# Optimization experiments

Hardware: AMD Instinct MI355X
Metric: run time of the kernel (lower is better)

The kernel has to match this reference:

```python
import jax, jax.numpy as jnp
import numpy as np

D_MODEL = 64
NUM_MODES = 16
SCALE = 1.0 / (D_MODEL * D_MODEL)


def setup_inputs() -> dict:
    key = jax.random.key(0)
    kq, kk, kv = jax.random.split(key, 3)
    shape = (4, 2048, 64, 64)  # (b, t, c, mw_dim)
    q = jax.random.normal(kq, shape, dtype=jnp.float32)
    k = jax.random.normal(kk, shape, dtype=jnp.float32)
    v = jax.random.normal(kv, shape, dtype=jnp.float32)
    return {"q": q, "k": k, "v": v}


def reference(q, k, v):
    b, t, c, mw = q.shape
    modes = min(t // 2, NUM_MODES)
    # permute (b,t,c,mw) -> (b,h,d,t) with h=mw_dim, d=c
    xq = jnp.transpose(q, (0, 3, 2, 1))
    xk = jnp.transpose(k, (0, 3, 2, 1))
    xv = jnp.transpose(v, (0, 3, 2, 1))
    # rfft over time, keep lowest `modes` frequency bins (contiguous low-pass)
    qf = jnp.fft.rfft(xq, axis=-1)[..., :modes]  # (b,h,d,modes) complex64
    kf = jnp.fft.rfft(xk, axis=-1)[..., :modes]
    vf = jnp.fft.rfft(xv, axis=-1)[..., :modes]
    # complex-domain attention over the reduced mode set
    qk = jnp.einsum('bhdx,bhdy->bhxy', qf, kf)  # (b,h,modes,modes)
    qk = jnp.tanh(qk)  # complex tanh, matching torch.tanh on cfloat
    qkv = jnp.einsum('bhxy,bhdy->bhdx', qk, vf)  # (b,h,d,modes)
    # scatter back into full rfft spectrum (zeros elsewhere)
    out_ft = jnp.zeros((b, mw, c, t // 2 + 1), dtype=qkv.dtype)
    out_ft = out_ft.at[..., :modes].set(qkv)
    out = jnp.fft.irfft(out_ft * SCALE, n=t, axis=-1)  # (b,h,d,t) float32
    return jnp.transpose(out, (0, 3, 2, 1))  # (b,t,c,mw)
```

## Files before the change

kernel.cpp:

```cpp
#include <hip/hip_runtime.h>
#include <hip/hip_bf16.h>
#include <math.h>


#define B_DIM 4
#define T_DIM 2048
#define DH 4096
#define MODES 16
#define CHUNKS 8
#define TPC (1024 / CHUNKS)

__global__ void init_tables(float* __restrict__ Wt, float* __restrict__ Bt) {
    int i = blockIdx.x * 256 + threadIdx.x;
    const float TWO_PI = 6.2831853071795864769f;
    if (i < 1024 * 32) {
        int t = i >> 5, j = i & 31, m = j & 15;
        int ph = (m * t) & 2047;
        float ang = TWO_PI * (float)ph / 2048.0f;
        Wt[i] = (j < 16) ? cosf(ang) : sinf(ang);
    }
    int i2 = i - 1024 * 32;
    if (i2 >= 0 && i2 < 2048 * 32) {
        int t = i2 >> 5, j = i2 & 31, m = j & 15;
        int ph = (m * t) & 2047;
        float ang = TWO_PI * (float)ph / 2048.0f;
        const float S2 = 1.0f / (4096.0f * 2048.0f);
        float coef = (m == 0 ? 1.0f : 2.0f) * S2;
        float val;
        if (j < 16)      val = coef * cosf(ang);
        else if (m == 0) val = 0.0f;
        else             val = -coef * sinf(ang);
        Bt[i2] = val;
    }
}

__global__ __launch_bounds__(256) void stageA(
        const float* __restrict__ q, const float* __restrict__ k,
        const float* __restrict__ v, const float* __restrict__ Wt,
        float* __restrict__ P) {
    int tid = threadIdx.x;
    int dh  = blockIdx.x * 256 + tid;
    int c   = blockIdx.y;
    int tz  = blockIdx.z;
    int tensor = tz >> 2;
    int b      = tz & 3;
    const float* src = (tensor == 0 ? q : tensor == 1 ? k : v)
                       + (size_t)b * T_DIM * DH;
    float accC[16], accS[16];
    #pragma unroll
    for (int m = 0; m < 16; m++) { accC[m] = 0.f; accS[m] = 0.f; }

    int t0 = c * TPC;
    const float* s0 = src + (size_t)t0 * DH + dh;
    const float* s1 = s0 + (size_t)1024 * DH;
    const float* wr0 = Wt + (size_t)t0 * 32;

    #pragma unroll 2
    for (int tl = 0; tl < TPC; tl++) {
        float x0 = s0[(size_t)tl * DH];
        float x1 = s1[(size_t)tl * DH];
        float u = x0 + x1;
        float w = x0 - x1;
        const float* wr = wr0 + tl * 32;
        #pragma unroll
        for (int m = 0; m < 16; m++) {
            float sm = (m & 1) ? w : u;
            accC[m] = fmaf(wr[m],      sm, accC[m]);
            accS[m] = fmaf(wr[16 + m], sm, accS[m]);
        }
    }
    float* pp = P + (((size_t)tz * CHUNKS + c) * 32) * DH + dh;
    #pragma unroll
    for (int m = 0; m < 16; m++) {
        pp[(size_t)m * DH]        = accC[m];
        pp[(size_t)(16 + m) * DH] = -accS[m];
    }
}

__global__ __launch_bounds__(256) void reduceP(const float* __restrict__ P,
                                               float* __restrict__ Y) {
    size_t i   = (size_t)blockIdx.x * 256 + threadIdx.x;
    size_t tzj = i >> 12;
    size_t dh  = i & 4095;
    size_t tz  = tzj >> 5;
    size_t j   = tzj & 31;
    const float* p = P + ((tz * CHUNKS) * 32 + j) * DH + dh;
    float s = 0.f;
    #pragma unroll
    for (int cc = 0; cc < CHUNKS; cc++) s += p[(size_t)cc * 32 * DH];
    Y[i] = s;
}

__global__ __launch_bounds__(256) void stageB(const float* __restrict__ Y,
                                              float* __restrict__ G) {
    __shared__ float qf[64 * 33];
    __shared__ float kf[64 * 33];
    __shared__ float vf[64 * 33];
    __shared__ float qkr[16 * 17];
    __shared__ float qki[16 * 17];

    int tid = threadIdx.x;
    int bh  = blockIdx.x;
    int b   = bh >> 6;
    int h   = bh & 63;

    #pragma unroll
    for (int tensor = 0; tensor < 3; tensor++) {
        float* dst = (tensor == 0 ? qf : tensor == 1 ? kf : vf);
        const float* yp = Y + ((size_t)(tensor * 4 + b) * 32) * DH + h;
        #pragma unroll
        for (int it = 0; it < 8; it++) {
            int p = it * 256 + tid;
            int d = p & 63, j = p >> 6;
            dst[d * 33 + j] = yp[(size_t)j * DH + d * 64];
        }
    }
    __syncthreads();

    int x = tid >> 4, y = tid & 15;
    float ar = 0.f, ai = 0.f;
    #pragma unroll 4
    for (int d = 0; d < 64; d++) {
        float qr = qf[d * 33 + x],      qi = qf[d * 33 + 16 + x];
        float kr = kf[d * 33 + y],      ki = kf[d * 33 + 16 + y];
        ar += qr * kr - qi * ki;
        ai += qr * ki + qi * kr;
    }
    float re, im;
    float a2 = 2.f * ar, b2 = 2.f * ai;
    if (fabsf(a2) < 80.f) {
        float den = coshf(a2) + cosf(b2);
        re = sinhf(a2) / den;
        im = sinf(b2) / den;
    } else {
        re = copysignf(1.f, ar);
        im = 0.f;
    }
    qkr[x * 17 + y] = re;
    qki[x * 17 + y] = im;
    __syncthreads();

    int xx = tid & 15, db = tid >> 4;
    #pragma unroll
    for (int i = 0; i < 4; i++) {
        int d = db + i * 16;
        float cr = 0.f, ci = 0.f;
        #pragma unroll
        for (int yy = 0; yy < 16; yy++) {
            float tr = qkr[xx * 17 + yy], ti = qki[xx * 17 + yy];
            float vr = vf[d * 33 + yy],   vi = vf[d * 33 + 16 + yy];
            cr += tr * vr - ti * vi;
            ci += tr * vi + ti * vr;
        }
        G[((size_t)b * 32 + xx) * DH + d * 64 + h]      = cr;
        G[((size_t)b * 32 + 16 + xx) * DH + d * 64 + h] = ci;
    }
}

__global__ __launch_bounds__(256) void stageC(const float* __restrict__ G,
                                              const float* __restrict__ Bt,
                                              float* __restrict__ out) {
    int tid   = threadIdx.x;
    int dh    = blockIdx.x * 256 + tid;
    int ttile = blockIdx.y;
    int b     = blockIdx.z;

    float g[32];
    const float* gp = G + (size_t)b * 32 * DH + dh;
    #pragma unroll
    for (int j = 0; j < 32; j++) g[j] = gp[(size_t)j * DH];

    float* op = out + ((size_t)b * T_DIM + (size_t)ttile * 128) * DH + dh;
    const float* bp = Bt + (size_t)ttile * 128 * 32;
    for (int tl = 0; tl < 128; tl++) {
        float acc = 0.f;
        #pragma unroll
        for (int j = 0; j < 32; j++) acc = fmaf(bp[tl * 32 + j], g[j], acc);
        op[(size_t)tl * DH] = acc;
    }
}

extern "C" void kernel_launch(void* const* d_in, const int* in_sizes, int n_in,
                              void* d_out, int out_size, void* d_ws, size_t ws_size,
                              hipStream_t stream) {
    const float* q = (const float*)d_in[0];
    const float* k = (const float*)d_in[1];
    const float* v = (const float*)d_in[2];
    float* out = (float*)d_out;

    char* ws = (char*)d_ws;
    float* Wt = (float*)ws;
    float* Bt = (float*)(ws + 131072);
    float* P  = (float*)(ws + 131072 + 262144);
    float* Y  = (float*)(ws + 131072 + 262144 + 50331648);
    float* G  = (float*)(ws + 131072 + 262144 + 50331648 + 6291456);

    init_tables<<<384, 256, 0, stream>>>(Wt, Bt);
    stageA<<<dim3(16, CHUNKS, 12), 256, 0, stream>>>(q, k, v, Wt, P);
    reduceP<<<6144, 256, 0, stream>>>(P, Y);
    stageB<<<256, 256, 0, stream>>>(Y, G);
    stageC<<<dim3(16, 16, 4), 256, 0, stream>>>(G, Bt, out);
}
```

Baseline: 463.9 us.

## Use radix-4 time folding, float2 vectorization and LDS twiddle tables in DFT stages

The forward DFT stage now folds the time axis four ways, using the periodicity of the low modes (m mod 4). This cuts the twiddle FMAs per sample, and each thread processes two channels with float2 loads. Twiddle tables are staged in shared memory rather than read from global memory, and the reduction kernel is vectorized to float4. The inverse stage uses even/odd mode symmetry to produce outputs at t and t+1024 from one accumulation, which halves its table work. In exchange, register pressure rises from float2 accumulators, there are fewer blocks, and the stage-A chunk length is shorter.

```diff
diff --git a/kernel.cpp b/kernel.cpp
--- a/kernel.cpp
+++ b/kernel.cpp
@@ -3,91 +3,124 @@
 #include <math.h>
 
 
-#define B_DIM 4
 #define T_DIM 2048
 #define DH 4096
-#define MODES 16
-#define CHUNKS 8
-#define TPC (1024 / CHUNKS)
-
-__global__ void init_tables(float* __restrict__ Wt, float* __restrict__ Bt) {
+#define DH2 2048
+#define CH 8
+#define TPCH 64
+#define TT 32
+
+__global__ void init_tables(float* __restrict__ WA, float* __restrict__ Bt2) {
     int i = blockIdx.x * 256 + threadIdx.x;
     const float TWO_PI = 6.2831853071795864769f;
-    if (i < 1024 * 32) {
-        int t = i >> 5, j = i & 31, m = j & 15;
+    if (i < 512 * 32) {
+        int t = i >> 5, r = i & 31, m = r >> 1;
         int ph = (m * t) & 2047;
-        float ang = TWO_PI * (float)ph / 2048.0f;
-        Wt[i] = (j < 16) ? cosf(ang) : sinf(ang);
-    }
-    int i2 = i - 1024 * 32;
-    if (i2 >= 0 && i2 < 2048 * 32) {
-        int t = i2 >> 5, j = i2 & 31, m = j & 15;
+        float ang = TWO_PI * (float)ph * (1.0f / 2048.0f);
+        WA[i] = (r & 1) ? sinf(ang) : cosf(ang);
+    }
+    int i2 = i - 512 * 32;
+    if (i2 >= 0 && i2 < 1024 * 32) {
+        int t = i2 >> 5, r = i2 & 31, m = r >> 1;
         int ph = (m * t) & 2047;
-        float ang = TWO_PI * (float)ph / 2048.0f;
+        float ang = TWO_PI * (float)ph * (1.0f / 2048.0f);
         const float S2 = 1.0f / (4096.0f * 2048.0f);
         float coef = (m == 0 ? 1.0f : 2.0f) * S2;
         float val;
-        if (j < 16)      val = coef * cosf(ang);
-        else if (m == 0) val = 0.0f;
-        else             val = -coef * sinf(ang);
-        Bt[i2] = val;
+        if (!(r & 1)) val = coef * cosf(ang);
+        else          val = (m == 0) ? 0.0f : -coef * sinf(ang);
+        Bt2[i2] = val;
     }
 }
 
 __global__ __launch_bounds__(256) void stageA(
         const float* __restrict__ q, const float* __restrict__ k,
-        const float* __restrict__ v, const float* __restrict__ Wt,
+        const float* __restrict__ v, const float* __restrict__ WA,
         float* __restrict__ P) {
+    __shared__ float w[TPCH * 32];
     int tid = threadIdx.x;
-    int dh  = blockIdx.x * 256 + tid;
     int c   = blockIdx.y;
     int tz  = blockIdx.z;
-    int tensor = tz >> 2;
-    int b      = tz & 3;
-    const float* src = (tensor == 0 ? q : tensor == 1 ? k : v)
-                       + (size_t)b * T_DIM * DH;
-    float accC[16], accS[16];
-    #pragma unroll
-    for (int m = 0; m < 16; m++) { accC[m] = 0.f; accS[m] = 0.f; }
-
-    int t0 = c * TPC;
-    const float* s0 = src + (size_t)t0 * DH + dh;
-    const float* s1 = s0 + (size_t)1024 * DH;
-    const float* wr0 = Wt + (size_t)t0 * 32;
+    int tensor = tz >> 2, b = tz & 3;
+
+    #pragma unroll
+    for (int it = 0; it < TPCH * 32 / 256; it++)
+        w[it * 256 + tid] = WA[c * (TPCH * 32) + it * 256 + tid];
+    __syncthreads();
+
+    int dh2 = blockIdx.x * 256 + tid;
+    const float* srcf = (tensor == 0 ? q : tensor == 1 ? k : v)
+                        + (size_t)b * T_DIM * DH;
+    const float2* p0 = (const float2*)srcf + (size_t)(c * TPCH) * DH2 + dh2;
+
+    float2 accR[16], accI[16];
+    #pragma unroll
+    for (int m = 0; m < 16; m++) {
+        accR[m] = make_float2(0.f, 0.f);
+        accI[m] = make_float2(0.f, 0.f);
+    }
 
     #pragma unroll 2
-    for (int tl = 0; tl < TPC; tl++) {
-        float x0 = s0[(size_t)tl * DH];
-        float x1 = s1[(size_t)tl * DH];
-        float u = x0 + x1;
-        float w = x0 - x1;
-        const float* wr = wr0 + tl * 32;
+    for (int tl = 0; tl < TPCH; tl++) {
+        float2 x0 = p0[(size_t)tl * DH2];
+        float2 x1 = p0[(size_t)(tl + 512) * DH2];
+        float2 x2 = p0[(size_t)(tl + 1024) * DH2];
+        float2 x3 = p0[(size_t)(tl + 1536) * DH2];
+        float2 u0 = make_float2(x0.x + x2.x, x0.y + x2.y);
+        float2 u1 = make_float2(x1.x + x3.x, x1.y + x3.y);
+        float2 d0 = make_float2(x0.x - x2.x, x0.y - x2.y);
+        float2 d1 = make_float2(x1.x - x3.x, x1.y - x3.y);
+        float2 e  = make_float2(u0.x + u1.x, u0.y + u1.y);
+        float2 f  = make_float2(u0.x - u1.x, u0.y - u1.y);
+        const float* ww = &w[tl * 32];
         #pragma unroll
         for (int m = 0; m < 16; m++) {
-            float sm = (m & 1) ? w : u;
-            accC[m] = fmaf(wr[m],      sm, accC[m]);
-            accS[m] = fmaf(wr[16 + m], sm, accS[m]);
-        }
-    }
-    float* pp = P + (((size_t)tz * CHUNKS + c) * 32) * DH + dh;
+            float cm = ww[2 * m], sm = ww[2 * m + 1];
+            if ((m & 3) == 0) {
+                accR[m].x = fmaf(cm, e.x, accR[m].x);
+                accR[m].y = fmaf(cm, e.y, accR[m].y);
+                accI[m].x = fmaf(-sm, e.x, accI[m].x);
+                accI[m].y = fmaf(-sm, e.y, accI[m].y);
+            } else if ((m & 3) == 2) {
+                accR[m].x = fmaf(cm, f.x, accR[m].x);
+                accR[m].y = fmaf(cm, f.y, accR[m].y);
+                accI[m].x = fmaf(-sm, f.x, accI[m].x);
+                accI[m].y = fmaf(-sm, f.y, accI[m].y);
+            } else if ((m & 3) == 1) {
+                accR[m].x = fmaf(cm, d0.x, fmaf(-sm, d1.x, accR[m].x));
+                accR[m].y = fmaf(cm, d0.y, fmaf(-sm, d1.y, accR[m].y));
+                accI[m].x = fmaf(-sm, d0.x, fmaf(-cm, d1.x, accI[m].x));
+                accI[m].y = fmaf(-sm, d0.y, fmaf(-cm, d1.y, accI[m].y));
+            } else {
+                accR[m].x = fmaf(cm, d0.x, fmaf(sm, d1.x, accR[m].x));
+                accR[m].y = fmaf(cm, d0.y, fmaf(sm, d1.y, accR[m].y));
+                accI[m].x = fmaf(-sm, d0.x, fmaf(cm, d1.x, accI[m].x));
+                accI[m].y = fmaf(-sm, d0.y, fmaf(cm, d1.y, accI[m].y));
+            }
+        }
+    }
+    float2* pp = (float2*)P + (((size_t)tz * CH + c) * 32) * DH2 + dh2;
     #pragma unroll
     for (int m = 0; m < 16; m++) {
-        pp[(size_t)m * DH]        = accC[m];
-        pp[(size_t)(16 + m) * DH] = -accS[m];
-    }
-}
-
-__global__ __launch_bounds__(256) void reduceP(const float* __restrict__ P,
-                                               float* __restrict__ Y) {
+        pp[(size_t)m * DH2]        = accR[m];
+        pp[(size_t)(16 + m) * DH2] = accI[m];
+    }
+}
+
+__global__ __launch_bounds__(256) void reduceP(const float4* __restrict__ P,
+                                               float4* __restrict__ Y) {
     size_t i   = (size_t)blockIdx.x * 256 + threadIdx.x;
-    size_t tzj = i >> 12;
-    size_t dh  = i & 4095;
+    size_t tzj = i >> 10;
+    size_t dh4 = i & 1023;
     size_t tz  = tzj >> 5;
     size_t j   = tzj & 31;
-    const float* p = P + ((tz * CHUNKS) * 32 + j) * DH + dh;
-    float s = 0.f;
-    #pragma unroll
-    for (int cc = 0; cc < CHUNKS; cc++) s += p[(size_t)cc * 32 * DH];
+    const float4* p = P + ((tz * CH) * 32 + j) * 1024 + dh4;
+    float4 s = make_float4(0.f, 0.f, 0.f, 0.f);
+    #pragma unroll
+    for (int cc = 0; cc < CH; cc++) {
+        float4 t = p[(size_t)cc * 32 * 1024];
+        s.x += t.x; s.y += t.y; s.z += t.z; s.w += t.w;
+    }
     Y[i] = s;
 }
 
@@ -158,25 +191,48 @@
 }
 
 __global__ __launch_bounds__(256) void stageC(const float* __restrict__ G,
-                                              const float* __restrict__ Bt,
+                                              const float* __restrict__ Bt2,
                                               float* __restrict__ out) {
-    int tid   = threadIdx.x;
-    int dh    = blockIdx.x * 256 + tid;
-    int ttile = blockIdx.y;
-    int b     = blockIdx.z;
-
-    float g[32];
-    const float* gp = G + (size_t)b * 32 * DH + dh;
-    #pragma unroll
-    for (int j = 0; j < 32; j++) g[j] = gp[(size_t)j * DH];
-
-    float* op = out + ((size_t)b * T_DIM + (size_t)ttile * 128) * DH + dh;
-    const float* bp = Bt + (size_t)ttile * 128 * 32;
-    for (int tl = 0; tl < 128; tl++) {
-        float acc = 0.f;
-        #pragma unroll
-        for (int j = 0; j < 32; j++) acc = fmaf(bp[tl * 32 + j], g[j], acc);
-        op[(size_t)tl * DH] = acc;
+    __shared__ float w[TT * 32];
+    int tid = threadIdx.x;
+    int c   = blockIdx.y;
+    int b   = blockIdx.z;
+
+    #pragma unroll
+    for (int it = 0; it < TT * 32 / 256; it++)
+        w[it * 256 + tid] = Bt2[c * (TT * 32) + it * 256 + tid];
+    __syncthreads();
+
+    int dh2 = blockIdx.x * 256 + tid;
+    float2 gr[16], gi[16];
+    const float2* gp = (const float2*)G + (size_t)b * 32 * DH2 + dh2;
+    #pragma unroll
+    for (int m = 0; m < 16; m++) {
+        gr[m] = gp[(size_t)m * DH2];
+        gi[m] = gp[(size_t)(16 + m) * DH2];
+    }
+
+    float2* o0 = (float2*)out + ((size_t)b * T_DIM + (size_t)c * TT) * DH2 + dh2;
+    #pragma unroll 2
+    for (int tl = 0; tl < TT; tl++) {
+        const float* ww = &w[tl * 32];
+        float2 E = make_float2(0.f, 0.f), O = make_float2(0.f, 0.f);
+        #pragma unroll
+        for (int m = 0; m < 16; m += 2) {
+            E.x = fmaf(ww[2 * m],     gr[m].x, E.x);
+            E.x = fmaf(ww[2 * m + 1], gi[m].x, E.x);
+            E.y = fmaf(ww[2 * m],     gr[m].y, E.y);
+            E.y = fmaf(ww[2 * m + 1], gi[m].y, E.y);
+        }
+        #pragma unroll
+        for (int m = 1; m < 16; m += 2) {
+            O.x = fmaf(ww[2 * m],     gr[m].x, O.x);
+            O.x = fmaf(ww[2 * m + 1], gi[m].x, O.x);
+            O.y = fmaf(ww[2 * m],     gr[m].y, O.y);
+            O.y = fmaf(ww[2 * m + 1], gi[m].y, O.y);
+        }
+        o0[(size_t)tl * DH2] = make_float2(E.x + O.x, E.y + O.y);
+        o0[(size_t)(tl + 1024) * DH2] = make_float2(E.x - O.x, E.y - O.y);
     }
 }
 
@@ -189,15 +245,15 @@
     float* out = (float*)d_out;
 
     char* ws = (char*)d_ws;
-    float* Wt = (float*)ws;
-    float* Bt = (float*)(ws + 131072);
-    float* P  = (float*)(ws + 131072 + 262144);
-    float* Y  = (float*)(ws + 131072 + 262144 + 50331648);
-    float* G  = (float*)(ws + 131072 + 262144 + 50331648 + 6291456);
-
-    init_tables<<<384, 256, 0, stream>>>(Wt, Bt);
-    stageA<<<dim3(16, CHUNKS, 12), 256, 0, stream>>>(q, k, v, Wt, P);
-    reduceP<<<6144, 256, 0, stream>>>(P, Y);
+    float* WA  = (float*)ws;
+    float* Bt2 = (float*)(ws + 65536);
+    float* P   = (float*)(ws + 65536 + 131072);
+    float* Y   = (float*)(ws + 65536 + 131072 + 50331648);
+    float* G   = (float*)(ws + 65536 + 131072 + 50331648 + 6291456);
+
+    init_tables<<<192, 256, 0, stream>>>(WA, Bt2);
+    stageA<<<dim3(8, CH, 12), 256, 0, stream>>>(q, k, v, WA, P);
+    reduceP<<<1536, 256, 0, stream>>>((const float4*)P, (float4*)Y);
     stageB<<<256, 256, 0, stream>>>(Y, G);
-    stageC<<<dim3(16, 16, 4), 256, 0, stream>>>(G, Bt, out);
-}
+    stageC<<<dim3(8, 32, 4), 256, 0, stream>>>(G, Bt2, out);
+}
```

Measured after the change: 451.7 us. -2.6%, faster.
